# Kernel tuning notes

Hardware: AMD Instinct MI355X
Metric: run time of the kernel (lower is better)

## Reference

```python
import jax, jax.numpy as jnp
import numpy as np

B, Q, D = 16, 1000, 256
HH, LV, NP = 8, 4, 4          # heads, levels, points per level
DH = D // HH                  # head dim = 32
TP = LV * NP                  # total points = 16
SHAPES = np.array([[64, 64], [32, 32], [16, 16], [8, 8]], dtype=np.int64)
LTOT = int((SHAPES[:, 0] * SHAPES[:, 1]).sum())  # 5440


def setup_inputs() -> dict:
    key = jax.random.key(0)
    ks = jax.random.split(key, 10)
    query = jax.random.normal(ks[0], (B, Q, D), dtype=jnp.float32)
    reference_points = jax.random.uniform(ks[1], (B, Q, LV, 2), dtype=jnp.float32)
    input_flatten = jax.random.normal(ks[2], (B, LTOT, D), dtype=jnp.float32)
    start = np.concatenate([[0], np.cumsum(SHAPES[:, 0] * SHAPES[:, 1])[:-1]])

    # params (mimic reset_parameters: directional bias init for offsets)
    thetas = np.arange(HH, dtype=np.float32) * (2.0 * np.pi / HH)
    grid = np.stack([np.cos(thetas), np.sin(thetas)], -1)
    grid = grid / np.abs(grid).max(-1, keepdims=True)
    grid = np.tile(grid[:, None, :], (1, TP, 1))  # [HH, TP, 2]
    scaling = np.concatenate([np.arange(1, NP + 1, dtype=np.float32) for _ in range(LV)]).reshape(1, TP, 1)
    bo = jnp.asarray((grid * scaling).reshape(-1), dtype=jnp.float32)

    s = 1.0 / np.sqrt(D)
    Wv = jax.random.normal(ks[3], (D, D), dtype=jnp.float32) * s
    bv = jnp.zeros((D,), dtype=jnp.float32)
    Wo = jax.random.normal(ks[4], (D, HH * TP * 2), dtype=jnp.float32) * 0.005
    Wa = jax.random.normal(ks[5], (D, HH * TP), dtype=jnp.float32) * 0.02
    ba = jnp.zeros((HH * TP,), dtype=jnp.float32)
    Wout = jax.random.normal(ks[6], (D, D), dtype=jnp.float32) * s
    bout = jnp.zeros((D,), dtype=jnp.float32)

    return {
        "query": query, "reference_points": reference_points, "input_flatten": input_flatten,
        "input_spatial_shapes": jnp.asarray(SHAPES), "input_level_start_index": jnp.asarray(start),
        "Wv": Wv, "bv": bv, "Wo": Wo, "bo": bo, "Wa": Wa, "ba": ba, "Wout": Wout, "bout": bout,
    }


def _sample_bilinear(val_flat, loc, Hl, Wl):
    # val_flat: [B, HH, DH, Hl*Wl]; loc: [B, Q, HH, p, 2] normalized in [0,1]
    # grid_sample align_corners=False, zeros padding: pixel = loc*size - 0.5
    b, q, h, p, _ = loc.shape
    x = loc[..., 0] * Wl - 0.5
    y = loc[..., 1] * Hl - 0.5
    x0 = jnp.floor(x); y0 = jnp.floor(y)
    lx = x - x0; ly = y - y0
    x0i = x0.astype(jnp.int32); y0i = y0.astype(jnp.int32)
    acc = jnp.zeros((b, h, val_flat.shape[2], q, p), dtype=val_flat.dtype)
    for ix, iy, w in ((x0i, y0i, (1 - lx) * (1 - ly)),
                      (x0i + 1, y0i, lx * (1 - ly)),
                      (x0i, y0i + 1, (1 - lx) * ly),
                      (x0i + 1, y0i + 1, lx * ly)):
        valid = ((ix >= 0) & (ix < Wl) & (iy >= 0) & (iy < Hl)).astype(val_flat.dtype)
        idx = jnp.clip(iy, 0, Hl - 1) * Wl + jnp.clip(ix, 0, Wl - 1)   # [B,Q,HH,p]
        idx = idx.transpose(0, 2, 1, 3).reshape(b, h, 1, q * p)
        v = jnp.take_along_axis(val_flat, idx, axis=3).reshape(b, h, -1, q, p)
        acc = acc + v * ((w * valid).transpose(0, 2, 1, 3)[:, :, None])
    return acc  # [B, HH, DH, Q, p]


def reference(query, reference_points, input_flatten, input_spatial_shapes,
              input_level_start_index, Wv, bv, Wo, bo, Wa, ba, Wout, bout):
    shapes = np.asarray(input_spatial_shapes)  # static level shapes
    shapes = shapes if shapes.any() else SHAPES  # fallback if zeros placeholder
    b, q, d = query.shape

    value = (input_flatten @ Wv + bv).reshape(b, -1, HH, DH)          # [B,L,HH,DH]
    off = (query @ Wo + bo).reshape(b, q, HH, LV, NP, 2)              # offsets
    attn = jax.nn.softmax((query @ Wa + ba).reshape(b, q, HH, TP), axis=-1)
    attn = attn.reshape(b, q, HH, LV, NP)

    # normalizer [LV,2] = (W_l, H_l)
    norm = jnp.stack([jnp.asarray(shapes[:, 1]), jnp.asarray(shapes[:, 0])], -1).astype(query.dtype)
    loc = reference_points[:, :, None, :, None, :] + off / norm[None, None, None, :, None, :]
    # loc: [B,Q,HH,LV,NP,2]

    out = jnp.zeros((b, HH, DH, q), dtype=query.dtype)
    start = 0
    for lvl in range(LV):
        Hl, Wl = int(shapes[lvl, 0]), int(shapes[lvl, 1])
        n = Hl * Wl
        val_l = value[:, start:start + n].transpose(0, 2, 3, 1)       # [B,HH,DH,n]
        start += n
        samp = _sample_bilinear(val_l, loc[:, :, :, lvl], Hl, Wl)     # [B,HH,DH,Q,NP]
        aw = attn[:, :, :, lvl].transpose(0, 2, 1, 3)                 # [B,HH,Q,NP]
        out = out + (samp * aw[:, :, None]).sum(-1)
    out = out.reshape(b, HH * DH, q).transpose(0, 2, 1)               # [B,Q,D]
    return out @ Wout + bout
```

## Files before the change

### kernel.cpp

```cpp
#include <hip/hip_runtime.h>

#define BB 16
#define QQ 1000
#define NH 8
#define LTOTAL 5440
#define MQ (BB*QQ)
#define MV (BB*LTOTAL)
#define NVBLK ((MV/128)*2)
#define NOBLK ((MQ/128)*3)

typedef __bf16 bf16x8 __attribute__((ext_vector_type(8)));
typedef float  f32x4  __attribute__((ext_vector_type(4)));

template <int N> struct IC { static constexpr int v = N; };

__device__ __forceinline__ unsigned short f2bf(float f) {
  unsigned u = __builtin_bit_cast(unsigned, f);
  u += 0x7fffu + ((u >> 16) & 1u);
  return (unsigned short)(u >> 16);
}
__device__ __forceinline__ float b2f_lo(unsigned u) {
  return __builtin_bit_cast(float, u << 16);
}
__device__ __forceinline__ float b2f_hi(unsigned u) {
  return __builtin_bit_cast(float, u & 0xffff0000u);
}

__device__ __forceinline__ void gload16(const void* g, void* l) {
  __builtin_amdgcn_global_load_lds(
      (const __attribute__((address_space(1))) unsigned int*)g,
      (__attribute__((address_space(3))) unsigned int*)l, 16, 0, 0);
}

__device__ __forceinline__ void pipe_barrier() {
  asm volatile("s_waitcnt lgkmcnt(0)" ::: "memory");
  __builtin_amdgcn_sched_barrier(0);
  __builtin_amdgcn_s_barrier();
  __builtin_amdgcn_sched_barrier(0);
}

__global__ __launch_bounds__(256) void prep_k(const float* __restrict__ Wv,
                                              const float* __restrict__ Wo,
                                              const float* __restrict__ Wa,
                                              const float* __restrict__ Wout,
                                              const float* __restrict__ bo,
                                              const float* __restrict__ ba,
                                              unsigned short* __restrict__ WvS,
                                              unsigned short* __restrict__ WcS,
                                              unsigned short* __restrict__ WoS,
                                              float* __restrict__ bcat) {
  int i = blockIdx.x * 256 + threadIdx.x;
  if (i < 28672) {
    const float* src;
    unsigned short* dst;
    int g, srcN;
    if (i < 8192)       { g = i;         dst = WvS; src = Wv;   srcN = 256; }
    else if (i < 20480) { g = i - 8192;  dst = WcS; src = Wo;   srcN = 256; }
    else                { g = i - 20480; dst = WoS; src = Wout; srcN = 256; }
    int panel = g >> 12, ko = (g >> 7) & 31, row = g & 127;
    int kbase = ko * 8;
    int n = panel * 128 + row;
    if (dst == WcS && panel == 2) { src = Wa; srcN = 128; n = row; }
    bf16x8 r;
#pragma unroll
    for (int e = 0; e < 8; e++) r[e] = (__bf16)src[(size_t)(kbase + e) * srcN + n];
    *(bf16x8*)(dst + (size_t)g * 8) = r;
  } else if (i < 29056) {
    int j = i - 28672;
    bcat[j] = j < 256 ? bo[j] : ba[j - 256];
  }
}

__global__ __launch_bounds__(256) void gemmf_k(const float* __restrict__ Aval,
                                               const float* __restrict__ Aoff,
                                               const unsigned short* __restrict__ WvS,
                                               const unsigned short* __restrict__ WcS,
                                               const float* __restrict__ bv,
                                               const float* __restrict__ bcat,
                                               unsigned short* __restrict__ Cval,
                                               float* __restrict__ Coff) {
  constexpr int K = 256, NT = 8;
  constexpr int STEADY = 6;
  constexpr int NWG = NVBLK + NOBLK;
  constexpr int QC = NWG / 8, RC = NWG % 8;
  __shared__ char lds[5 * 8192];
  char* As = lds;
  char* Bs = lds + 2 * 8192;

  int orig = blockIdx.x;
  int xcd = orig & 7, pos = orig >> 3;
  int bid = (xcd < RC ? xcd * (QC + 1) : RC * (QC + 1) + (xcd - RC) * QC) + pos;

  bool isVal = bid < NVBLK;
  int vbid = isVal ? bid : bid - NVBLK;
  int ntiles = isVal ? 2 : 3;
  const float* Av = isVal ? Aval : Aoff;
  const unsigned short* WS = isVal ? WvS : WcS;
  const float* bias = isVal ? bv : bcat;

  int tid = threadIdx.x, wave = tid >> 6, lane = tid & 63;
  int mt = vbid / ntiles, nt = vbid - mt * ntiles;
  int r16 = lane & 15, kg = lane >> 4;
  int wm = wave >> 1, wn = wave & 1;
  int arow = tid >> 1, ahalf = tid & 1;

  const unsigned short* Bpanel = WS + (size_t)nt * (NT * 512 * 8);
  const float* Ag32 = Av + (size_t)(mt * 128 + arow) * K + ahalf * 16;

  f32x4 ar[2][4];
  f32x4 acc[4][4] = {};

  auto stageB = [&](int s) {
    char* Bd = Bs + (s % 3) * 8192;
    const unsigned short* sp = Bpanel + (size_t)s * 512 * 8;
#pragma unroll
    for (int j = 0; j < 2; j++) {
      int f = (j * 4 + wave) * 64 + lane;
      gload16(sp + f * 8, Bd + f * 16);
    }
  };
  auto loadA32 = [&](int s, f32x4* r) {
    const float* sp = Ag32 + s * 32;
    r[0] = *(const f32x4*)(sp);
    r[1] = *(const f32x4*)(sp + 4);
    r[2] = *(const f32x4*)(sp + 8);
    r[3] = *(const f32x4*)(sp + 12);
  };
  auto writeA32 = [&](int slot, f32x4* r) {
    bf16x8 g0, g1;
    g0[0]=(__bf16)r[0][0]; g0[1]=(__bf16)r[0][1]; g0[2]=(__bf16)r[0][2]; g0[3]=(__bf16)r[0][3];
    g0[4]=(__bf16)r[1][0]; g0[5]=(__bf16)r[1][1]; g0[6]=(__bf16)r[1][2]; g0[7]=(__bf16)r[1][3];
    g1[0]=(__bf16)r[2][0]; g1[1]=(__bf16)r[2][1]; g1[2]=(__bf16)r[2][2]; g1[3]=(__bf16)r[2][3];
    g1[4]=(__bf16)r[3][0]; g1[5]=(__bf16)r[3][1]; g1[6]=(__bf16)r[3][2]; g1[7]=(__bf16)r[3][3];
    char* Ad = As + slot * 8192;
    int u0 = ahalf * 2;
    *(bf16x8*)(Ad + (((u0    ) * 128 + arow) << 4)) = g0;
    *(bf16x8*)(Ad + (((u0 + 1) * 128 + arow) << 4)) = g1;
  };
  auto compute = [&](int sa, int sb) {
    const char* Ad = As + sa * 8192;
    const char* Bd = Bs + sb * 8192;
    bf16x8 af[4], bq[4];
#pragma unroll
    for (int mi = 0; mi < 4; mi++) {
      int row = wm * 64 + mi * 16 + r16;
      af[mi] = *(const bf16x8*)(Ad + ((kg * 128 + row) << 4));
    }
#pragma unroll
    for (int ni = 0; ni < 4; ni++) {
      int row = wn * 64 + ni * 16 + r16;
      bq[ni] = *(const bf16x8*)(Bd + ((kg * 128 + row) << 4));
    }
#pragma unroll
    for (int mi = 0; mi < 4; mi++)
#pragma unroll
      for (int ni = 0; ni < 4; ni++)
        acc[mi][ni] = __builtin_amdgcn_mfma_f32_16x16x32_bf16(bq[ni], af[mi], acc[mi][ni], 0, 0, 0);
  };

  loadA32(0, ar[0]); stageB(0); loadA32(1, ar[1]); stageB(1);
  writeA32(0, ar[0]);
  asm volatile("s_waitcnt vmcnt(%0)" :: "i"(STEADY) : "memory");
  pipe_barrier();

  auto step = [&](auto TC) {
    constexpr int t = decltype(TC)::v;
    if constexpr (t + 2 < NT) {
      loadA32(t + 2, ar[(t + 2) & 1]);
      stageB(t + 2);
    }
    compute(t & 1, t % 3);
    if constexpr (t + 1 < NT) {
      writeA32((t + 1) & 1, ar[(t + 1) & 1]);
      if constexpr (t + 2 < NT)
        asm volatile("s_waitcnt vmcnt(%0)" :: "i"(STEADY) : "memory");
      else
        asm volatile("s_waitcnt vmcnt(0)" ::: "memory");
      pipe_barrier();
    }
  };
  step(IC<0>{}); step(IC<1>{}); step(IC<2>{}); step(IC<3>{});
  step(IC<4>{}); step(IC<5>{}); step(IC<6>{}); step(IC<7>{});

  int rowBase = mt * 128 + wm * 64;
  int colBase = nt * 128 + wn * 64;
#pragma unroll
  for (int ni = 0; ni < 4; ni++) {
    int col = colBase + ni * 16 + kg * 4;
    f32x4 bs = *(const f32x4*)(bias + col);
#pragma unroll
    for (int mi = 0; mi < 4; mi++) {
      int row = rowBase + mi * 16 + r16;
      f32x4 v = acc[mi][ni] + bs;
      if (isVal) {
        uint2 st;
        st.x = f2bf(v[0]) | ((unsigned)f2bf(v[1]) << 16);
        st.y = f2bf(v[2]) | ((unsigned)f2bf(v[3]) << 16);
        *(uint2*)(Cval + (size_t)row * 256 + col) = st;
      } else {
        *(f32x4*)(Coff + (size_t)row * 384 + col) = v;
      }
    }
  }
}

__global__ __launch_bounds__(256) void gemm3b_k(const unsigned short* __restrict__ Av,
                                                const unsigned short* __restrict__ WS,
                                                const float* __restrict__ bias,
                                                float* __restrict__ C, int M, int N) {
  constexpr int NT = 8;
  constexpr int STEADY = 4;
  __shared__ char lds[6 * 8192];
  char* As = lds;
  char* Bs = lds + 3 * 8192;

  int tid = threadIdx.x, wave = tid >> 6, lane = tid & 63;
  int ntiles = N >> 7;
  int mt = blockIdx.x / ntiles, nt = blockIdx.x - (blockIdx.x / ntiles) * ntiles;
  int r16 = lane & 15, kg = lane >> 4;
  int wm = wave >> 1, wn = wave & 1;

  const unsigned short* Bpanel = WS + (size_t)nt * (NT * 512 * 8);
  const unsigned short* Apanel = Av + (size_t)mt * (NT * 512 * 8);

  f32x4 acc[4][4] = {};

  auto stageB = [&](int s) {
    char* Bd = Bs + (s % 3) * 8192;
    const unsigned short* sp = Bpanel + (size_t)s * 512 * 8;
#pragma unroll
    for (int j = 0; j < 2; j++) {
      int f = (j * 4 + wave) * 64 + lane;
      gload16(sp + f * 8, Bd + f * 16);
    }
  };
  auto stageA16 = [&](int s) {
    char* Ad = As + (s % 3) * 8192;
    const unsigned short* sp = Apanel + (size_t)s * 512 * 8;
#pragma unroll
    for (int j = 0; j < 2; j++) {
      int f = (j * 4 + wave) * 64 + lane;
      gload16(sp + f * 8, Ad + f * 16);
    }
  };
  auto compute = [&](int s) {
    const char* Ad = As + (s % 3) * 8192;
    const char* Bd = Bs + (s % 3) * 8192;
    bf16x8 af[4], bq[4];
#pragma unroll
    for (int mi = 0; mi < 4; mi++) {
      int row = wm * 64 + mi * 16 + r16;
      af[mi] = *(const bf16x8*)(Ad + ((kg * 128 + row) << 4));
    }
#pragma unroll
    for (int ni = 0; ni < 4; ni++) {
      int row = wn * 64 + ni * 16 + r16;
      bq[ni] = *(const bf16x8*)(Bd + ((kg * 128 + row) << 4));
    }
#pragma unroll
    for (int mi = 0; mi < 4; mi++)
#pragma unroll
      for (int ni = 0; ni < 4; ni++)
        acc[mi][ni] = __builtin_amdgcn_mfma_f32_16x16x32_bf16(bq[ni], af[mi], acc[mi][ni], 0, 0, 0);
  };

  stageA16(0); stageB(0); stageA16(1); stageB(1);
  asm volatile("s_waitcnt vmcnt(%0)" :: "i"(STEADY) : "memory");
  pipe_barrier();

  auto step = [&](auto TC) {
    constexpr int t = decltype(TC)::v;
    if constexpr (t + 2 < NT) { stageA16(t + 2); stageB(t + 2); }
    compute(t);
    if constexpr (t + 1 < NT) {
      if constexpr (t + 2 < NT)
        asm volatile("s_waitcnt vmcnt(%0)" :: "i"(STEADY) : "memory");
      else
        asm volatile("s_waitcnt vmcnt(0)" ::: "memory");
      pipe_barrier();
    }
  };
  step(IC<0>{}); step(IC<1>{}); step(IC<2>{}); step(IC<3>{});
  step(IC<4>{}); step(IC<5>{}); step(IC<6>{}); step(IC<7>{});

  int rowBase = mt * 128 + wm * 64;
  int colBase = nt * 128 + wn * 64;
#pragma unroll
  for (int ni = 0; ni < 4; ni++) {
    int col = colBase + ni * 16 + kg * 4;
    f32x4 bs = *(const f32x4*)(bias + col);
#pragma unroll
    for (int mi = 0; mi < 4; mi++) {
      int row = rowBase + mi * 16 + r16;
      f32x4 v = acc[mi][ni] + bs;
      *(f32x4*)(C + (size_t)row * N + col) = v;
    }
  }
}

__global__ __launch_bounds__(256, 3) void sample_k(const float* __restrict__ offattn,
                                                   const float* __restrict__ refp,
                                                   const unsigned short* __restrict__ value,
                                                   unsigned short* __restrict__ interS) {
  int orig = blockIdx.x;
  int sb = (orig & 7) * 250 + (orig >> 3);
  int t  = sb * 256 + threadIdx.x;
  int bq = t >> 5;
  int h  = (t >> 2) & 7;
  int c0 = (t & 3) << 3;
  int b  = bq / QQ;

  const float* base = offattn + (size_t)bq * 384;

  float lg[16];
  const float4* ab4 = (const float4*)(base + 256 + h * 16);
#pragma unroll
  for (int i = 0; i < 4; i++) {
    float4 v = ab4[i];
    lg[4*i] = v.x; lg[4*i+1] = v.y; lg[4*i+2] = v.z; lg[4*i+3] = v.w;
  }
  float m = -1e30f;
#pragma unroll
  for (int i = 0; i < 16; i++) m = fmaxf(m, lg[i]);
  float s = 0.f;
#pragma unroll
  for (int i = 0; i < 16; i++) { lg[i] = __expf(lg[i] - m); s += lg[i]; }
  float inv = 1.0f / s;

  float4 r01 = ((const float4*)(refp + (size_t)bq * 8))[0];
  float4 r23 = ((const float4*)(refp + (size_t)bq * 8))[1];
  float rxs[4] = {r01.x, r01.z, r23.x, r23.z};
  float rys[4] = {r01.y, r01.w, r23.y, r23.w};

  const unsigned short* vb = value + (size_t)b * (LTOTAL * 256) + h * 32 + c0;
  const int startL[4] = {0, 4096, 5120, 5376};

  float acc[8] = {};
#pragma unroll
  for (int lvl = 0; lvl < 4; lvl++) {
    int   Wi = 64 >> lvl;
    float Wf = (float)Wi;
    float px = rxs[lvl] * Wf - 0.5f;
    float py = rys[lvl] * Wf - 0.5f;
    const unsigned short* vl = vb + (size_t)startL[lvl] * 256;

    const float4* ob4 = (const float4*)(base + h * 32 + lvl * 8);
    float4 o01 = ob4[0], o23 = ob4[1];
    float oxs[4] = {o01.x, o01.z, o23.x, o23.z};
    float oys[4] = {o01.y, o01.w, o23.y, o23.w};

    float cw[16];
    int   coff[16];
#pragma unroll
    for (int pt = 0; pt < 4; pt++) {
      float wa = lg[lvl * 4 + pt] * inv;
      float x = px + oxs[pt];
      float y = py + oys[pt];
      float xf = floorf(x), yf = floorf(y);
      float lx = x - xf, ly = y - yf;
      int x0 = (int)xf, y0 = (int)yf;
      float wx[2] = {1.f - lx, lx};
      float wy[2] = {1.f - ly, ly};
#pragma unroll
      for (int cy = 0; cy < 2; cy++) {
        int Y = y0 + cy;
        bool vy = (unsigned)Y < (unsigned)Wi;
        int Yc = min(max(Y, 0), Wi - 1);
#pragma unroll
        for (int cx = 0; cx < 2; cx++) {
          int X = x0 + cx;
          bool vx = (unsigned)X < (unsigned)Wi;
          int Xc = min(max(X, 0), Wi - 1);
          int c = pt * 4 + cy * 2 + cx;
          cw[c]   = (vx && vy) ? wa * wy[cy] * wx[cx] : 0.f;
          coff[c] = (Yc * Wi + Xc) * 256;
        }
      }
    }
    uint4 raw[16];
#pragma unroll
    for (int c = 0; c < 16; c++) raw[c] = *(const uint4*)(vl + coff[c]);
#pragma unroll
    for (int c = 0; c < 16; c++) {
      float w = cw[c];
      acc[0] += w * b2f_lo(raw[c].x); acc[1] += w * b2f_hi(raw[c].x);
      acc[2] += w * b2f_lo(raw[c].y); acc[3] += w * b2f_hi(raw[c].y);
      acc[4] += w * b2f_lo(raw[c].z); acc[5] += w * b2f_hi(raw[c].z);
      acc[6] += w * b2f_lo(raw[c].w); acc[7] += w * b2f_hi(raw[c].w);
    }
  }

  unsigned o0 = f2bf(acc[0]) | ((unsigned)f2bf(acc[1]) << 16);
  unsigned o1 = f2bf(acc[2]) | ((unsigned)f2bf(acc[3]) << 16);
  unsigned o2 = f2bf(acc[4]) | ((unsigned)f2bf(acc[5]) << 16);
  unsigned o3 = f2bf(acc[6]) | ((unsigned)f2bf(acc[7]) << 16);
  uint4 st = {o0, o1, o2, o3};

  int mtile = bq >> 7, row = bq & 127;
  size_t goff = (((size_t)(mtile * 8 + h)) * 512 + (c0 >> 3) * 128 + row) * 8;
  *(uint4*)(interS + goff) = st;
}

extern "C" void kernel_launch(void* const* d_in, const int* in_sizes, int n_in,
                              void* d_out, int out_size, void* d_ws, size_t ws_size,
                              hipStream_t stream) {
  const float* query  = (const float*)d_in[0];
  const float* refp   = (const float*)d_in[1];
  const float* inputf = (const float*)d_in[2];
  const float* Wv   = (const float*)d_in[5];
  const float* bv   = (const float*)d_in[6];
  const float* Wo   = (const float*)d_in[7];
  const float* bo   = (const float*)d_in[8];
  const float* Wa   = (const float*)d_in[9];
  const float* ba   = (const float*)d_in[10];
  const float* Wout = (const float*)d_in[11];
  const float* bout = (const float*)d_in[12];

  char* p = (char*)d_ws;
  auto alloc = [&](size_t bytes) -> char* {
    char* r = p;
    p += (bytes + 255) & ~(size_t)255;
    return r;
  };
  unsigned short* val   = (unsigned short*)alloc((size_t)MV * 256 * 2);
  unsigned short* WvS   = (unsigned short*)alloc(2 * 4096 * 8 * 2);
  unsigned short* WcS   = (unsigned short*)alloc(3 * 4096 * 8 * 2);
  unsigned short* WoS   = (unsigned short*)alloc(2 * 4096 * 8 * 2);
  float*          bcat  = (float*)alloc(384 * 4);
  float*          offattn = (float*)alloc((size_t)MQ * 384 * 4);
  unsigned short* interS = (unsigned short*)alloc((size_t)MQ * 256 * 2);

  prep_k<<<114, 256, 0, stream>>>(Wv, Wo, Wa, Wout, bo, ba, WvS, WcS, WoS, bcat);

  gemmf_k<<<NVBLK + NOBLK, 256, 0, stream>>>(inputf, query, WvS, WcS, bv, bcat,
                                             val, offattn);
  sample_k<<<MQ * 32 / 256, 256, 0, stream>>>(offattn, refp, val, interS);
  gemm3b_k<<<(MQ / 128) * 2, 256, 0, stream>>>(interS, WoS, bout, (float*)d_out,
                                               MQ, 256);
}
```

Measured before the change: 89.27 us.

## Stage weight tiles through registers with three-deep prefetch instead of direct LDS loads

The fused projection GEMM stops using direct global-to-LDS loads for the B (weight) tiles. Both A and B stages are now prefetched into registers three stages ahead and written to double-buffered LDS. This cuts LDS from 40KB to 32KB and adds a launch-bounds occupancy hint of 3 blocks per CU. The trade-off is more register pressure from the extra staging arrays, and the explicit vmcnt waits are replaced by compiler-managed dependencies.

```diff
diff --git a/kernel.cpp b/kernel.cpp
--- a/kernel.cpp
+++ b/kernel.cpp
@@ -71,19 +71,18 @@
   }
 }
 
-__global__ __launch_bounds__(256) void gemmf_k(const float* __restrict__ Aval,
-                                               const float* __restrict__ Aoff,
-                                               const unsigned short* __restrict__ WvS,
-                                               const unsigned short* __restrict__ WcS,
-                                               const float* __restrict__ bv,
-                                               const float* __restrict__ bcat,
-                                               unsigned short* __restrict__ Cval,
-                                               float* __restrict__ Coff) {
+__global__ __launch_bounds__(256, 3) void gemmf_k(const float* __restrict__ Aval,
+                                                  const float* __restrict__ Aoff,
+                                                  const unsigned short* __restrict__ WvS,
+                                                  const unsigned short* __restrict__ WcS,
+                                                  const float* __restrict__ bv,
+                                                  const float* __restrict__ bcat,
+                                                  unsigned short* __restrict__ Cval,
+                                                  float* __restrict__ Coff) {
   constexpr int K = 256, NT = 8;
-  constexpr int STEADY = 6;
   constexpr int NWG = NVBLK + NOBLK;
   constexpr int QC = NWG / 8, RC = NWG % 8;
-  __shared__ char lds[5 * 8192];
+  __shared__ char lds[4 * 8192];
   char* As = lds;
   char* Bs = lds + 2 * 8192;
 
@@ -107,39 +106,38 @@
   const unsigned short* Bpanel = WS + (size_t)nt * (NT * 512 * 8);
   const float* Ag32 = Av + (size_t)(mt * 128 + arow) * K + ahalf * 16;
 
-  f32x4 ar[2][4];
-  f32x4 acc[4][4] = {};
-
-  auto stageB = [&](int s) {
-    char* Bd = Bs + (s % 3) * 8192;
-    const unsigned short* sp = Bpanel + (size_t)s * 512 * 8;
-#pragma unroll
-    for (int j = 0; j < 2; j++) {
-      int f = (j * 4 + wave) * 64 + lane;
-      gload16(sp + f * 8, Bd + f * 16);
-    }
-  };
-  auto loadA32 = [&](int s, f32x4* r) {
+  f32x4  ar[3][4];
+  bf16x8 br[3][2];
+  f32x4  acc[4][4] = {};
+
+  auto loadStage = [&](int s, int slot) {
     const float* sp = Ag32 + s * 32;
-    r[0] = *(const f32x4*)(sp);
-    r[1] = *(const f32x4*)(sp + 4);
-    r[2] = *(const f32x4*)(sp + 8);
-    r[3] = *(const f32x4*)(sp + 12);
-  };
-  auto writeA32 = [&](int slot, f32x4* r) {
+    ar[slot][0] = *(const f32x4*)(sp);
+    ar[slot][1] = *(const f32x4*)(sp + 4);
+    ar[slot][2] = *(const f32x4*)(sp + 8);
+    ar[slot][3] = *(const f32x4*)(sp + 12);
+    const unsigned short* bp = Bpanel + (size_t)s * 512 * 8;
+    br[slot][0] = *(const bf16x8*)(bp + (size_t)tid * 8);
+    br[slot][1] = *(const bf16x8*)(bp + (size_t)(tid + 256) * 8);
+  };
+  auto writeStage = [&](int s, int slot) {
+    f32x4* r = ar[slot];
     bf16x8 g0, g1;
     g0[0]=(__bf16)r[0][0]; g0[1]=(__bf16)r[0][1]; g0[2]=(__bf16)r[0][2]; g0[3]=(__bf16)r[0][3];
     g0[4]=(__bf16)r[1][0]; g0[5]=(__bf16)r[1][1]; g0[6]=(__bf16)r[1][2]; g0[7]=(__bf16)r[1][3];
     g1[0]=(__bf16)r[2][0]; g1[1]=(__bf16)r[2][1]; g1[2]=(__bf16)r[2][2]; g1[3]=(__bf16)r[2][3];
     g1[4]=(__bf16)r[3][0]; g1[5]=(__bf16)r[3][1]; g1[6]=(__bf16)r[3][2]; g1[7]=(__bf16)r[3][3];
-    char* Ad = As + slot * 8192;
+    char* Ad = As + (s & 1) * 8192;
     int u0 = ahalf * 2;
     *(bf16x8*)(Ad + (((u0    ) * 128 + arow) << 4)) = g0;
     *(bf16x8*)(Ad + (((u0 + 1) * 128 + arow) << 4)) = g1;
-  };
-  auto compute = [&](int sa, int sb) {
-    const char* Ad = As + sa * 8192;
-    const char* Bd = Bs + sb * 8192;
+    char* Bd = Bs + (s & 1) * 8192;
+    *(bf16x8*)(Bd + (size_t)tid * 16) = br[slot][0];
+    *(bf16x8*)(Bd + (size_t)(tid + 256) * 16) = br[slot][1];
+  };
+  auto compute = [&](int t) {
+    const char* Ad = As + (t & 1) * 8192;
+    const char* Bd = Bs + (t & 1) * 8192;
     bf16x8 af[4], bq[4];
 #pragma unroll
     for (int mi = 0; mi < 4; mi++) {
@@ -158,24 +156,16 @@
         acc[mi][ni] = __builtin_amdgcn_mfma_f32_16x16x32_bf16(bq[ni], af[mi], acc[mi][ni], 0, 0, 0);
   };
 
-  loadA32(0, ar[0]); stageB(0); loadA32(1, ar[1]); stageB(1);
-  writeA32(0, ar[0]);
-  asm volatile("s_waitcnt vmcnt(%0)" :: "i"(STEADY) : "memory");
+  loadStage(0, 0); loadStage(1, 1); loadStage(2, 2);
+  writeStage(0, 0);
   pipe_barrier();
 
   auto step = [&](auto TC) {
     constexpr int t = decltype(TC)::v;
-    if constexpr (t + 2 < NT) {
-      loadA32(t + 2, ar[(t + 2) & 1]);
-      stageB(t + 2);
-    }
-    compute(t & 1, t % 3);
+    if constexpr (t + 3 < NT) loadStage(t + 3, (t + 3) % 3);
+    compute(t);
     if constexpr (t + 1 < NT) {
-      writeA32((t + 1) & 1, ar[(t + 1) & 1]);
-      if constexpr (t + 2 < NT)
-        asm volatile("s_waitcnt vmcnt(%0)" :: "i"(STEADY) : "memory");
-      else
-        asm volatile("s_waitcnt vmcnt(0)" ::: "memory");
+      writeStage(t + 1, (t + 1) % 3);
       pipe_barrier();
     }
   };
```

Result: slower. 101.6 us (+13.8%).

## Split fused projection GEMM into a full-width value GEMM and a separate offset GEMM

Applied to the files above, without the earlier changes.

The combined value/offset GEMM kernel is split in two. The value projection becomes its own 512-thread kernel whose 128x256 tile covers the full N width, so each fp32 input row is read and converted to bf16 once instead of twice. The offset/attention GEMM keeps the old tiling in a separate launch. This adds one more kernel launch, removes the overlap the fused grid gave between the two GEMMs, and uses more LDS per block, which may lower occupancy.

```diff
diff --git a/kernel.cpp b/kernel.cpp
--- a/kernel.cpp
+++ b/kernel.cpp
@@ -6,8 +6,6 @@
 #define LTOTAL 5440
 #define MQ (BB*QQ)
 #define MV (BB*LTOTAL)
-#define NVBLK ((MV/128)*2)
-#define NOBLK ((MQ/128)*3)
 
 typedef __bf16 bf16x8 __attribute__((ext_vector_type(8)));
 typedef float  f32x4  __attribute__((ext_vector_type(4)));
@@ -71,17 +69,121 @@
   }
 }
 
-__global__ __launch_bounds__(256) void gemmf_k(const float* __restrict__ Aval,
-                                               const float* __restrict__ Aoff,
+__global__ __launch_bounds__(512) void gemmv_k(const float* __restrict__ Av,
                                                const unsigned short* __restrict__ WvS,
+                                               const float* __restrict__ bias,
+                                               unsigned short* __restrict__ C) {
+  constexpr int K = 256, NT = 8;
+  __shared__ char lds[2 * 8192 + 3 * 16384];
+  char* As = lds;
+  char* Bs = lds + 16384;
+
+  int orig = blockIdx.x;
+  int mt = (orig & 7) * 85 + (orig >> 3);
+
+  int tid = threadIdx.x, wave = tid >> 6, lane = tid & 63;
+  int r16 = lane & 15, kg = lane >> 4;
+  int wm = wave >> 2, wn = wave & 3;
+  int arow = tid >> 2, au = tid & 3;
+
+  const float* Ag32 = Av + (size_t)(mt * 128 + arow) * K + au * 8;
+
+  f32x4 ar[2][2];
+  f32x4 acc[4][4] = {};
+
+  auto loadA = [&](int s, int slot) {
+    const float* sp = Ag32 + s * 32;
+    ar[slot][0] = *(const f32x4*)(sp);
+    ar[slot][1] = *(const f32x4*)(sp + 4);
+  };
+  auto writeA = [&](int s, int slot) {
+    f32x4 lo = ar[slot][0], hi = ar[slot][1];
+    bf16x8 g;
+    g[0]=(__bf16)lo[0]; g[1]=(__bf16)lo[1]; g[2]=(__bf16)lo[2]; g[3]=(__bf16)lo[3];
+    g[4]=(__bf16)hi[0]; g[5]=(__bf16)hi[1]; g[6]=(__bf16)hi[2]; g[7]=(__bf16)hi[3];
+    char* Ad = As + (s & 1) * 8192;
+    *(bf16x8*)(Ad + ((au * 128 + arow) << 4)) = g;
+  };
+  auto stageB = [&](int s) {
+    char* Bd = Bs + (s % 3) * 16384;
+#pragma unroll
+    for (int j = 0; j < 2; j++) {
+      int f = j * 512 + tid;
+      int u = f >> 8, col = f & 255;
+      const unsigned short* sp = WvS +
+          ((size_t)(col >> 7) * 4096 + (size_t)(s * 4 + u) * 128 + (col & 127)) * 8;
+      gload16(sp, Bd + (size_t)f * 16);
+    }
+  };
+  auto compute = [&](int t) {
+    const char* Ad = As + (t & 1) * 8192;
+    const char* Bd = Bs + (t % 3) * 16384;
+    bf16x8 af[4], bq[4];
+#pragma unroll
+    for (int mi = 0; mi < 4; mi++) {
+      int row = wm * 64 + mi * 16 + r16;
+      af[mi] = *(const bf16x8*)(Ad + ((kg * 128 + row) << 4));
+    }
+#pragma unroll
+    for (int ni = 0; ni < 4; ni++) {
+      int col = wn * 64 + ni * 16 + r16;
+      bq[ni] = *(const bf16x8*)(Bd + ((kg * 256 + col) << 4));
+    }
+#pragma unroll
+    for (int mi = 0; mi < 4; mi++)
+#pragma unroll
+      for (int ni = 0; ni < 4; ni++)
+        acc[mi][ni] = __builtin_amdgcn_mfma_f32_16x16x32_bf16(bq[ni], af[mi], acc[mi][ni], 0, 0, 0);
+  };
+
+  loadA(0, 0); stageB(0); loadA(1, 1); stageB(1);
+  writeA(0, 0);
+  asm volatile("s_waitcnt vmcnt(4)" ::: "memory");
+  pipe_barrier();
+
+  auto step = [&](auto TC) {
+    constexpr int t = decltype(TC)::v;
+    if constexpr (t + 2 < NT) {
+      loadA(t + 2, t & 1);
+      stageB(t + 2);
+    }
+    compute(t);
+    if constexpr (t + 1 < NT) {
+      writeA(t + 1, (t + 1) & 1);
+      if constexpr (t + 2 < NT)
+        asm volatile("s_waitcnt vmcnt(4)" ::: "memory");
+      else
+        asm volatile("s_waitcnt vmcnt(0)" ::: "memory");
+      pipe_barrier();
+    }
+  };
+  step(IC<0>{}); step(IC<1>{}); step(IC<2>{}); step(IC<3>{});
+  step(IC<4>{}); step(IC<5>{}); step(IC<6>{}); step(IC<7>{});
+
+  int rowBase = mt * 128 + wm * 64;
+  int colBase = wn * 64;
+#pragma unroll
+  for (int ni = 0; ni < 4; ni++) {
+    int col = colBase + ni * 16 + kg * 4;
+    f32x4 bs = *(const f32x4*)(bias + col);
+#pragma unroll
+    for (int mi = 0; mi < 4; mi++) {
+      int row = rowBase + mi * 16 + r16;
+      f32x4 v = acc[mi][ni] + bs;
+      uint2 st;
+      st.x = f2bf(v[0]) | ((unsigned)f2bf(v[1]) << 16);
+      st.y = f2bf(v[2]) | ((unsigned)f2bf(v[3]) << 16);
+      *(uint2*)(C + (size_t)row * 256 + col) = st;
+    }
+  }
+}
+
+__global__ __launch_bounds__(256) void gemmo_k(const float* __restrict__ Av,
                                                const unsigned short* __restrict__ WcS,
-                                               const float* __restrict__ bv,
-                                               const float* __restrict__ bcat,
-                                               unsigned short* __restrict__ Cval,
+                                               const float* __restrict__ bias,
                                                float* __restrict__ Coff) {
   constexpr int K = 256, NT = 8;
-  constexpr int STEADY = 6;
-  constexpr int NWG = NVBLK + NOBLK;
+  constexpr int NWG = (MQ / 128) * 3;
   constexpr int QC = NWG / 8, RC = NWG % 8;
   __shared__ char lds[5 * 8192];
   char* As = lds;
@@ -91,20 +193,13 @@
   int xcd = orig & 7, pos = orig >> 3;
   int bid = (xcd < RC ? xcd * (QC + 1) : RC * (QC + 1) + (xcd - RC) * QC) + pos;
 
-  bool isVal = bid < NVBLK;
-  int vbid = isVal ? bid : bid - NVBLK;
-  int ntiles = isVal ? 2 : 3;
-  const float* Av = isVal ? Aval : Aoff;
-  const unsigned short* WS = isVal ? WvS : WcS;
-  const float* bias = isVal ? bv : bcat;
-
   int tid = threadIdx.x, wave = tid >> 6, lane = tid & 63;
-  int mt = vbid / ntiles, nt = vbid - mt * ntiles;
+  int mt = bid / 3, nt = bid - mt * 3;
   int r16 = lane & 15, kg = lane >> 4;
   int wm = wave >> 1, wn = wave & 1;
   int arow = tid >> 1, ahalf = tid & 1;
 
-  const unsigned short* Bpanel = WS + (size_t)nt * (NT * 512 * 8);
+  const unsigned short* Bpanel = WcS + (size_t)nt * (NT * 512 * 8);
   const float* Ag32 = Av + (size_t)(mt * 128 + arow) * K + ahalf * 16;
 
   f32x4 ar[2][4];
@@ -160,7 +255,7 @@
 
   loadA32(0, ar[0]); stageB(0); loadA32(1, ar[1]); stageB(1);
   writeA32(0, ar[0]);
-  asm volatile("s_waitcnt vmcnt(%0)" :: "i"(STEADY) : "memory");
+  asm volatile("s_waitcnt vmcnt(6)" ::: "memory");
   pipe_barrier();
 
   auto step = [&](auto TC) {
@@ -173,7 +268,7 @@
     if constexpr (t + 1 < NT) {
       writeA32((t + 1) & 1, ar[(t + 1) & 1]);
       if constexpr (t + 2 < NT)
-        asm volatile("s_waitcnt vmcnt(%0)" :: "i"(STEADY) : "memory");
+        asm volatile("s_waitcnt vmcnt(6)" ::: "memory");
       else
         asm volatile("s_waitcnt vmcnt(0)" ::: "memory");
       pipe_barrier();
@@ -192,14 +287,7 @@
     for (int mi = 0; mi < 4; mi++) {
       int row = rowBase + mi * 16 + r16;
       f32x4 v = acc[mi][ni] + bs;
-      if (isVal) {
-        uint2 st;
-        st.x = f2bf(v[0]) | ((unsigned)f2bf(v[1]) << 16);
-        st.y = f2bf(v[2]) | ((unsigned)f2bf(v[3]) << 16);
-        *(uint2*)(Cval + (size_t)row * 256 + col) = st;
-      } else {
-        *(f32x4*)(Coff + (size_t)row * 384 + col) = v;
-      }
+      *(f32x4*)(Coff + (size_t)row * 384 + col) = v;
     }
   }
 }
@@ -432,8 +520,8 @@
 
   prep_k<<<114, 256, 0, stream>>>(Wv, Wo, Wa, Wout, bo, ba, WvS, WcS, WoS, bcat);
 
-  gemmf_k<<<NVBLK + NOBLK, 256, 0, stream>>>(inputf, query, WvS, WcS, bv, bcat,
-                                             val, offattn);
+  gemmv_k<<<MV / 128, 512, 0, stream>>>(inputf, WvS, bv, val);
+  gemmo_k<<<(MQ / 128) * 3, 256, 0, stream>>>(query, WcS, bcat, offattn);
   sample_k<<<MQ * 32 / 256, 256, 0, stream>>>(offattn, refp, val, interS);
   gemm3b_k<<<(MQ / 128) * 2, 256, 0, stream>>>(interS, WoS, bout, (float*)d_out,
                                                MQ, 256);
```

New measurement: 94.07 us. 1.05x slower.
